# Performance work log

Measured on AMD Instinct MI355X. Metric: run time of the kernel, lower is better.

## Reference

```python
import jax, jax.numpy as jnp
import numpy as np

T, B, N, E, NF, L = 4, 8, 5000, 80000, 16, 3


def setup_inputs() -> dict:
    key = jax.random.key(0)
    ks = jax.random.split(key, 12)
    xs = jax.random.normal(ks[0], (T, B, N, 3), jnp.float32)
    vs = jax.random.normal(ks[1], (T, B, N, 3), jnp.float32)
    charges = jax.random.uniform(ks[2], (B * N, 1), jnp.float32)
    edge_src = jax.random.randint(ks[3], (E,), 0, N)
    edge_dst = jax.random.randint(ks[4], (E,), 0, N)
    theta = jax.random.uniform(ks[5], (1, T), jnp.float32, -1.0, 1.0)  # uniform_(-1,1)
    W_embed = jax.random.normal(ks[6], (1, NF), jnp.float32) * 0.5
    W1 = jax.random.normal(ks[7], (L, 2 * NF + 1, NF), jnp.float32) / jnp.sqrt(2.0 * NF + 1)
    b1 = jnp.zeros((L, NF), jnp.float32)
    W2 = jax.random.normal(ks[8], (L, NF, NF), jnp.float32) / jnp.sqrt(float(NF))
    b2 = jnp.zeros((L, NF), jnp.float32)
    Wv = jax.random.normal(ks[9], (L, NF, 1), jnp.float32) * 0.1
    return dict(xs=xs, vs=vs, charges=charges, edge_src=edge_src, edge_dst=edge_dst,
                theta=theta, W_embed=W_embed, W1=W1, b1=b1, W2=W2, b2=b2, Wv=Wv)


def reference(xs, vs, charges, edge_src, edge_dst, theta, W_embed, W1, b1, W2, b2, Wv):
    T_, B_, N_, _ = xs.shape
    # node scalar features ('f' / type-0) initialized from charges
    h0 = jax.nn.relu(charges.reshape(B_, N_, 1) @ W_embed)  # [B, N, NF]

    def graph_step(x, v, h):
        # x, v: [N,3]; h: [N,NF]. Equivariant message passing with edge rel-pos gather.
        d = x[edge_dst] - x[edge_src]                      # [E,3]  (edata['d'])
        d2 = jnp.sum(d * d, axis=-1, keepdims=True)        # [E,1]  invariant edge feature
        vec = v                                            # type-1 ('vel') channel
        for l in range(L):
            feat = jnp.concatenate([h[edge_src], h[edge_dst], d2], axis=-1)  # [E,2NF+1]
            m = jax.nn.relu(feat @ W1[l] + b1[l])                            # [E,NF]
            agg = jax.ops.segment_sum(m, edge_dst, num_segments=N_)          # [N,NF]
            h = h + jax.nn.relu(agg @ W2[l] + b2[l])
            # equivariant vector update: scatter d-weighted messages
            vec = vec + jax.ops.segment_sum(d * (m @ Wv[l]), edge_dst, num_segments=N_)
        return vec + x  # module returns out + xs

    step_b = jax.vmap(graph_step)                                  # over batch
    out = jax.vmap(lambda x, v: step_b(x, v, h0))(xs, vs)          # [T,B,N,3]
    x = out.reshape(T_, B_ * N_, 3)                                # step's view(-1, 3)
    x_hat = jnp.einsum('ij,jkt->ikt', jax.nn.softmax(theta, axis=1), x)
    return x_hat.squeeze(0)  # [B*N, 3] since num_future == 1
```

## Files before the change

kernel.cpp:

```cpp
#include <hip/hip_runtime.h>
#include <hip/hip_bf16.h>

constexpr int T_ = 4;
constexpr int B_ = 8;
constexpr int N_ = 5000;
constexpr int E_ = 80000;
constexpr int TBN = T_ * B_ * N_;
constexpr int NXCD = 8;
constexpr int CAP = 64;

constexpr int NPB = 32;
constexpr int CH  = (N_ + NPB - 1) / NPB;
constexpr int GRP = T_ * B_ / NXCD;
constexpr int LB  = NXCD * CH * GRP;
constexpr int EB  = (E_ + 255) / 256;
constexpr int IB  = TBN / 256;


typedef _Float16 h2 __attribute__((ext_vector_type(2)));
__device__ __forceinline__ unsigned h2u(h2 v) {
    union { h2 h; unsigned u; } x; x.h = v; return x.u;
}
__device__ __forceinline__ h2 u2h(unsigned u) {
    union { h2 h; unsigned u; } x; x.u = u; return x.h;
}
__device__ __forceinline__ unsigned f16pack2(float lo, float hi) {
    auto v = __builtin_amdgcn_cvt_pkrtz(lo, hi);
    union { decltype(v) h; unsigned u; } x; x.h = v; return x.u;
}
__device__ __forceinline__ void f16unpack2(unsigned u, float& lo, float& hi) {
    h2 v = u2h(u); lo = (float)v[0]; hi = (float)v[1];
}

__global__ void k_build(const int* __restrict__ src, const int* __restrict__ dst,
                        int* __restrict__ cursor, unsigned short* __restrict__ csr_b,
                        const float* __restrict__ xs, const float* __restrict__ vs,
                        const float* __restrict__ charges,
                        float4* __restrict__ rec0, float4* __restrict__ rec1,
                        float* __restrict__ vec) {
    const int bid = blockIdx.x;
    const int tid = threadIdx.x;
    if (bid < EB) {
        int e = bid * 256 + tid;
        if (e < E_) {
            int d = dst[e];
            int pos = atomicAdd(&cursor[d], 1);
            if (pos < CAP) csr_b[d * CAP + pos] = (unsigned short)src[e];
        }
    } else {
        int g = (bid - EB) * 256 + tid;
        int tb = g / N_;
        int n  = g - tb * N_;
        int b  = tb % B_;
        float c = charges[b * N_ + n];
        float4 xc = make_float4(xs[3*(size_t)g], xs[3*(size_t)g+1], xs[3*(size_t)g+2], c);
        rec0[(size_t)g * 3 + 2] = xc;
        rec1[(size_t)g * 3 + 2] = xc;
        vec[3*(size_t)g+0] = vs[3*(size_t)g+0];
        vec[3*(size_t)g+1] = vs[3*(size_t)g+1];
        vec[3*(size_t)g+2] = vs[3*(size_t)g+2];
    }
}

template <int LYR, bool HAS_NEXT>
__global__ __launch_bounds__(256, 6) void k_layer(
        const float4* __restrict__ rec_in, float4* __restrict__ rec_out,
        const float* __restrict__ W_embed,
        const float* __restrict__ W1, const float* __restrict__ b1,
        const float* __restrict__ W2, const float* __restrict__ b2,
        const float* __restrict__ Wv, const float* __restrict__ theta,
        const int* __restrict__ degv, const unsigned short* __restrict__ csr_b,
        unsigned* __restrict__ hbuf, unsigned* __restrict__ gd,
        float* __restrict__ vec, float* __restrict__ outp) {
    __shared__ float s_w1e[16], s_wv[16], s_b2[16], s_b1[16], s_b1n[16];
    __shared__ float s_W2[256];
    __shared__ float s_W1sn[256];
    __shared__ float s_W1dn[256];
    __shared__ float s_P[16], s_Q[16], s_rwe[16];
    const int tid = threadIdx.x;
    if (tid < 16) {
        s_w1e[tid] = W1[LYR * 528 + 512 + tid];
        s_wv[tid]  = Wv[LYR * 16 + tid];
        s_b2[tid]  = b2[LYR * 16 + tid];
        s_b1[tid]  = b1[LYR * 16 + tid];
        if (HAS_NEXT) s_b1n[tid] = b1[(LYR + 1) * 16 + tid];
    }
    s_W2[tid] = W2[LYR * 256 + tid];
    if (HAS_NEXT) {
        s_W1sn[tid] = W1[(LYR + 1) * 528 + tid];
        s_W1dn[tid] = W1[(LYR + 1) * 528 + 256 + tid];
    }
    if (LYR == 0 && tid < 16) {
        float accP = 0.0f, accQ = 0.0f;
        for (int j = 0; j < 16; ++j) {
            float r = fmaxf(W_embed[j], 0.0f);
            accP += r * W1[j * 16 + tid];
            accQ += r * W1[256 + j * 16 + tid];
        }
        s_P[tid] = accP; s_Q[tid] = accQ;
        s_rwe[tid] = fmaxf(W_embed[tid], 0.0f);
    }
    __syncthreads();

    const int bid   = blockIdx.x;
    const int xcd   = bid & 7;
    const int j     = bid >> 3;
    const int tb    = xcd + NXCD * (j / CH);
    const int chunk = j % CH;
    const int o     = tid & 7;
    const int node  = chunk * NPB + (tid >> 3);
    const int half  = o & 1;
    const int pr    = o >> 1;
    const int hb    = half * 8;
    if (node >= N_) return;

    const int g = tb * N_ + node;
    const size_t nb = (size_t)tb * N_;
    const uint4* r4 = (const uint4*)rec_in;

    float wsm = 0.0f;
    if (!HAS_NEXT) {
        float t0 = theta[0], t1 = theta[1], t2 = theta[2], t3 = theta[3];
        float mx = fmaxf(fmaxf(t0, t1), fmaxf(t2, t3));
        float e0 = expf(t0 - mx), e1 = expf(t1 - mx);
        float e2 = expf(t2 - mx), e3 = expf(t3 - mx);
        float inv = 1.0f / (e0 + e1 + e2 + e3);
        int tt = tb >> 3;
        wsm = ((tt == 0) ? e0 : (tt == 1) ? e1 : (tt == 2) ? e2 : e3) * inv;
    }

    const float4 xn = rec_in[(size_t)g * 3 + 2];
    const float c0 = xn.w;

    h2 w1e_pk[4], wv_pk[4], P_pk[4];
#pragma unroll
    for (int k = 0; k < 4; ++k) {
        w1e_pk[k] = u2h(f16pack2(s_w1e[hb + 2*k], s_w1e[hb + 2*k + 1]));
        wv_pk[k]  = u2h(f16pack2(s_wv[hb + 2*k],  s_wv[hb + 2*k + 1]));
        if (LYR == 0) P_pk[k] = u2h(f16pack2(s_P[hb + 2*k], s_P[hb + 2*k + 1]));
    }

    h2 gdn_pk[4];
    if (LYR == 0) {
#pragma unroll
        for (int k = 0; k < 4; ++k)
            gdn_pk[k] = u2h(f16pack2(c0 * s_Q[hb + 2*k]     + s_b1[hb + 2*k],
                                     c0 * s_Q[hb + 2*k + 1] + s_b1[hb + 2*k + 1]));
    } else {
        uint4 da = ((const uint4*)gd)[(size_t)g * 2 + half];
        gdn_pk[0] = u2h(da.x); gdn_pk[1] = u2h(da.y);
        gdn_pk[2] = u2h(da.z); gdn_pk[3] = u2h(da.w);
    }

    const h2 h2z = {(_Float16)0.0f, (_Float16)0.0f};
    h2 agg_pk[4] = {h2z, h2z, h2z, h2z};
    float av0 = 0.0f, av1 = 0.0f, av2 = 0.0f;

    const int deg = min(degv[node], CAP);
    const int rs = node * CAP;
    const int re = rs + deg;

    int e = rs + pr;
    bool have = e < re;
    int s = have ? (int)csr_b[e] : 0;
    size_t si = nb + (size_t)s;
    float4 xc = rec_in[si * 3 + 2];
    uint4  ga;
    if (LYR != 0) ga = r4[si * 3 + half];

    while (have) {
        int e2 = e + 4;
        bool have2 = e2 < re;
        int s2 = have2 ? (int)csr_b[e2] : 0;
        size_t si2 = nb + (size_t)s2;
        float4 xc2 = rec_in[si2 * 3 + 2];
        uint4  ga2;
        if (LYR != 0) ga2 = r4[si2 * 3 + half];

        float d0 = xn.x - xc.x;
        float d1 = xn.y - xc.y;
        float d2v = xn.z - xc.z;
        float dd = d0*d0 + d1*d1 + d2v*d2v;
        _Float16 ddh = (_Float16)dd;
        h2 dd2 = {ddh, ddh};
        h2 cs2 = h2z;
        if (LYR == 0) { _Float16 ch = (_Float16)xc.w; cs2 = (h2){ch, ch}; }

        h2 sv = h2z;
#pragma unroll
        for (int k = 0; k < 4; ++k) {
            h2 gsk;
            if (LYR == 0) gsk = cs2 * P_pk[k];
            else gsk = u2h(k == 0 ? ga.x : (k == 1 ? ga.y : (k == 2 ? ga.z : ga.w)));
            h2 m = dd2 * w1e_pk[k] + gdn_pk[k] + gsk;
            m = __builtin_elementwise_max(m, h2z);
            if (HAS_NEXT) agg_pk[k] += m;
            sv = m * wv_pk[k] + sv;
        }
        float sval = (float)sv[0] + (float)sv[1];
        sval += __shfl_xor(sval, 1);
        av0 = __builtin_fmaf(d0, sval, av0);
        av1 = __builtin_fmaf(d1, sval, av1);
        av2 = __builtin_fmaf(d2v, sval, av2);

        e = e2; have = have2; xc = xc2; ga = ga2;
    }

    av0 += __shfl_xor(av0, 2); av0 += __shfl_xor(av0, 4);
    av1 += __shfl_xor(av1, 2); av1 += __shfl_xor(av1, 4);
    av2 += __shfl_xor(av2, 2); av2 += __shfl_xor(av2, 4);

    if (HAS_NEXT) {
        if (o < 3) {
            float myav = (o == 0) ? av0 : ((o == 1) ? av1 : av2);
            vec[(size_t)g * 3 + o] += myav;
        }

        float agg[8], aggO[8];
#pragma unroll
        for (int k = 0; k < 4; ++k) {
            agg_pk[k] += u2h(__shfl_xor(h2u(agg_pk[k]), 2));
            agg_pk[k] += u2h(__shfl_xor(h2u(agg_pk[k]), 4));
            unsigned po = __shfl_xor(h2u(agg_pk[k]), 1);
            h2 v = agg_pk[k], vo = u2h(po);
            agg[2*k]   = (float)v[0];  agg[2*k+1]  = (float)v[1];
            aggO[2*k]  = (float)vo[0]; aggO[2*k+1] = (float)vo[1];
        }
        const int j0 = hb;
        const int j1 = 8 - hb;

        float hq0, hq1;
        if (LYR == 0) {
            hq0 = c0 * s_rwe[o * 2];
            hq1 = c0 * s_rwe[o * 2 + 1];
        } else {
            f16unpack2(hbuf[(size_t)g * 8 + o], hq0, hq1);
        }

        float a0 = s_b2[o * 2], a1 = s_b2[o * 2 + 1];
#pragma unroll
        for (int k = 0; k < 8; ++k) {
            a0 = __builtin_fmaf(agg[k],  s_W2[(j0 + k) * 16 + o * 2],     a0);
            a1 = __builtin_fmaf(agg[k],  s_W2[(j0 + k) * 16 + o * 2 + 1], a1);
            a0 = __builtin_fmaf(aggO[k], s_W2[(j1 + k) * 16 + o * 2],     a0);
            a1 = __builtin_fmaf(aggO[k], s_W2[(j1 + k) * 16 + o * 2 + 1], a1);
        }
        hq0 += fmaxf(a0, 0.0f);
        hq1 += fmaxf(a1, 0.0f);

        const int lane = tid & 63;
        const int lbase = lane & ~7;
        float hfull[16];
#pragma unroll
        for (int sq = 0; sq < 8; ++sq) {
            hfull[sq * 2]     = __shfl(hq0, lbase + sq, 64);
            hfull[sq * 2 + 1] = __shfl(hq1, lbase + sq, 64);
        }

        float gs0 = 0.0f, gs1 = 0.0f;
        float gd0 = s_b1n[o * 2], gd1 = s_b1n[o * 2 + 1];
#pragma unroll
        for (int jj = 0; jj < 16; ++jj) {
            float hj = hfull[jj];
            gs0 = __builtin_fmaf(hj, s_W1sn[jj * 16 + o * 2],     gs0);
            gs1 = __builtin_fmaf(hj, s_W1sn[jj * 16 + o * 2 + 1], gs1);
            gd0 = __builtin_fmaf(hj, s_W1dn[jj * 16 + o * 2],     gd0);
            gd1 = __builtin_fmaf(hj, s_W1dn[jj * 16 + o * 2 + 1], gd1);
        }

        hbuf[(size_t)g * 8 + o] = f16pack2(hq0, hq1);
        ((unsigned*)rec_out)[(size_t)g * 12 + o] = f16pack2(gs0, gs1);
        ((unsigned*)gd)[(size_t)g * 8 + o]       = f16pack2(gd0, gd1);
    } else {
        if (o < 3) {
            float myav = (o == 0) ? av0 : ((o == 1) ? av1 : av2);
            float xno  = (o == 0) ? xn.x : ((o == 1) ? xn.y : xn.z);
            float prev = vec[(size_t)g * 3 + o];
            int b = tb & 7;
            atomicAdd(&outp[((size_t)b * N_ + node) * 3 + o],
                      wsm * (prev + myav + xno));
        }
    }
}

extern "C" void kernel_launch(void* const* d_in, const int* in_sizes, int n_in,
                              void* d_out, int out_size, void* d_ws, size_t ws_size,
                              hipStream_t stream) {
    const float* xs       = (const float*)d_in[0];
    const float* vs       = (const float*)d_in[1];
    const float* charges  = (const float*)d_in[2];
    const int*   edge_src = (const int*)d_in[3];
    const int*   edge_dst = (const int*)d_in[4];
    const float* theta    = (const float*)d_in[5];
    const float* W_embed  = (const float*)d_in[6];
    const float* W1       = (const float*)d_in[7];
    const float* b1       = (const float*)d_in[8];
    const float* W2       = (const float*)d_in[9];
    const float* b2       = (const float*)d_in[10];
    const float* Wv       = (const float*)d_in[11];
    float* out = (float*)d_out;

    char* w = (char*)d_ws;
    size_t off = 0;
    auto take = [&](size_t bytes) {
        size_t o = off;
        off = (off + bytes + 255) & ~(size_t)255;
        return o;
    };
    int*            cursor = (int*)(w + take((size_t)N_ * 4));
    unsigned short* csr_b  = (unsigned short*)(w + take((size_t)N_ * CAP * 2));
    float4*         rec0   = (float4*)(w + take((size_t)TBN * 48));
    float4*         rec1   = (float4*)(w + take((size_t)TBN * 48));
    unsigned*       hbuf   = (unsigned*)(w + take((size_t)TBN * 32));
    unsigned*       gd     = (unsigned*)(w + take((size_t)TBN * 32));
    float*          vec    = (float*)(w + take((size_t)TBN * 3 * 4));
    (void)ws_size;

    hipMemsetAsync(cursor, 0, (size_t)N_ * 4, stream);
    hipMemsetAsync(out, 0, (size_t)out_size * 4, stream);
    k_build<<<EB + IB, 256, 0, stream>>>(edge_src, edge_dst, cursor, csr_b,
                                         xs, vs, charges, rec0, rec1, vec);

    k_layer<0, true ><<<LB, 256, 0, stream>>>(rec0, rec1, W_embed, W1, b1, W2, b2, Wv,
                                              theta, cursor, csr_b, hbuf, gd, vec, out);
    k_layer<1, true ><<<LB, 256, 0, stream>>>(rec1, rec0, W_embed, W1, b1, W2, b2, Wv,
                                              theta, cursor, csr_b, hbuf, gd, vec, out);
    k_layer<2, false><<<LB, 256, 0, stream>>>(rec0, nullptr, W_embed, W1, b1, W2, b2, Wv,
                                              theta, cursor, csr_b, hbuf, gd, vec, out);
}
```

Baseline: 100.1 us.

## Issue first eight neighbor gathers unconditionally with masking; fold output zeroing into build kernel

Replaces the software-pipelined while loop over each node's neighbors with a contiguous per-lane chunk in which the first eight source indices and their record gathers are issued together up front. Lanes past their valid count use clamped indices and a zero mask on the message, so more loads are in flight at once. The output memset is also removed and the zeroing is done inside the build kernel, saving one launch. The cost is extra wasted gathers and ALU work for low-degree nodes, plus reads of possibly uninitialized CSR slots that are clamped and masked.

```diff
diff --git a/kernel.cpp b/kernel.cpp
--- a/kernel.cpp
+++ b/kernel.cpp
@@ -37,7 +37,7 @@
                         const float* __restrict__ xs, const float* __restrict__ vs,
                         const float* __restrict__ charges,
                         float4* __restrict__ rec0, float4* __restrict__ rec1,
-                        float* __restrict__ vec) {
+                        float* __restrict__ vec, float4* __restrict__ outz) {
     const int bid = blockIdx.x;
     const int tid = threadIdx.x;
     if (bid < EB) {
@@ -59,6 +59,7 @@
         vec[3*(size_t)g+0] = vs[3*(size_t)g+0];
         vec[3*(size_t)g+1] = vs[3*(size_t)g+1];
         vec[3*(size_t)g+2] = vs[3*(size_t)g+2];
+        if (g < (B_ * N_ * 3) / 4) outz[g] = make_float4(0.f, 0.f, 0.f, 0.f);
     }
 }
 
@@ -158,25 +159,12 @@
 
     const int deg = min(degv[node], CAP);
     const int rs = node * CAP;
-    const int re = rs + deg;
-
-    int e = rs + pr;
-    bool have = e < re;
-    int s = have ? (int)csr_b[e] : 0;
-    size_t si = nb + (size_t)s;
-    float4 xc = rec_in[si * 3 + 2];
-    uint4  ga;
-    if (LYR != 0) ga = r4[si * 3 + half];
-
-    while (have) {
-        int e2 = e + 4;
-        bool have2 = e2 < re;
-        int s2 = have2 ? (int)csr_b[e2] : 0;
-        size_t si2 = nb + (size_t)s2;
-        float4 xc2 = rec_in[si2 * 3 + 2];
-        uint4  ga2;
-        if (LYR != 0) ga2 = r4[si2 * 3 + half];
-
+
+    const int q   = (deg + 3) >> 2;
+    const int my0 = pr * q;
+    const int myn = max(0, min(q, deg - my0));
+
+    auto edge = [&](const float4& xc, const uint4& ga, float mk) {
         float d0 = xn.x - xc.x;
         float d1 = xn.y - xc.y;
         float d2v = xn.z - xc.z;
@@ -185,6 +173,8 @@
         h2 dd2 = {ddh, ddh};
         h2 cs2 = h2z;
         if (LYR == 0) { _Float16 ch = (_Float16)xc.w; cs2 = (h2){ch, ch}; }
+        _Float16 mh = (_Float16)mk;
+        h2 mk2 = {mh, mh};
 
         h2 sv = h2z;
 #pragma unroll
@@ -194,6 +184,7 @@
             else gsk = u2h(k == 0 ? ga.x : (k == 1 ? ga.y : (k == 2 ? ga.z : ga.w)));
             h2 m = dd2 * w1e_pk[k] + gdn_pk[k] + gsk;
             m = __builtin_elementwise_max(m, h2z);
+            m = m * mk2;
             if (HAS_NEXT) agg_pk[k] += m;
             sv = m * wv_pk[k] + sv;
         }
@@ -202,8 +193,37 @@
         av0 = __builtin_fmaf(d0, sval, av0);
         av1 = __builtin_fmaf(d1, sval, av1);
         av2 = __builtin_fmaf(d2v, sval, av2);
-
-        e = e2; have = have2; xc = xc2; ga = ga2;
+    };
+
+    {
+        const int kn = min(myn, 8);
+        int s0 = min((int)csr_b[rs + my0 + 0], N_ - 1);
+        int s1 = min((int)csr_b[rs + my0 + 1], N_ - 1);
+        int s2 = min((int)csr_b[rs + my0 + 2], N_ - 1);
+        int s3 = min((int)csr_b[rs + my0 + 3], N_ - 1);
+        int s4 = min((int)csr_b[rs + my0 + 4], N_ - 1);
+        int s5 = min((int)csr_b[rs + my0 + 5], N_ - 1);
+        int s6 = min((int)csr_b[rs + my0 + 6], N_ - 1);
+        int s7 = min((int)csr_b[rs + my0 + 7], N_ - 1);
+        int sx[8] = {s0, s1, s2, s3, s4, s5, s6, s7};
+#pragma unroll
+        for (int k = 0; k < 8; ++k) {
+            size_t si = nb + (size_t)sx[k];
+            float4 xc = rec_in[si * 3 + 2];
+            uint4  ga = {0, 0, 0, 0};
+            if (LYR != 0) ga = r4[si * 3 + half];
+            edge(xc, ga, (k < kn) ? 1.0f : 0.0f);
+        }
+    }
+    if (myn > 8) {
+        for (int k = 8; k < myn; ++k) {
+            int s = min((int)csr_b[rs + my0 + k], N_ - 1);
+            size_t si = nb + (size_t)s;
+            float4 xc = rec_in[si * 3 + 2];
+            uint4  ga = {0, 0, 0, 0};
+            if (LYR != 0) ga = r4[si * 3 + half];
+            edge(xc, ga, 1.0f);
+        }
     }
 
     av0 += __shfl_xor(av0, 2); av0 += __shfl_xor(av0, 4);
@@ -317,9 +337,9 @@
     (void)ws_size;
 
     hipMemsetAsync(cursor, 0, (size_t)N_ * 4, stream);
-    hipMemsetAsync(out, 0, (size_t)out_size * 4, stream);
     k_build<<<EB + IB, 256, 0, stream>>>(edge_src, edge_dst, cursor, csr_b,
-                                         xs, vs, charges, rec0, rec1, vec);
+                                         xs, vs, charges, rec0, rec1, vec,
+                                         (float4*)out);
 
     k_layer<0, true ><<<LB, 256, 0, stream>>>(rec0, rec1, W_embed, W1, b1, W2, b2, Wv,
                                               theta, cursor, csr_b, hbuf, gd, vec, out);
```

Result: slower. 125.1 us (+24.9%).
